# Performance work log

Hardware: AMD Instinct MI355X
Metric: run time of the kernel (lower is better)

## Reference

```python
import jax, jax.numpy as jnp
import numpy as np
from jax import lax

NT, TL = 32, 64           # num_trajs, traj_length
H, W, C = 84, 84, 4       # Atari frame stack
SIZE = 256                # LSTM hidden size
NOUT = 18                 # num_outputs
FEAT = 6 * 6 * 32         # after four stride-2 SAME convs: 84->42->21->11->6
DN = ('NHWC', 'HWIO', 'NHWC')


def setup_inputs() -> dict:
    key = jax.random.key(0)
    ks = jax.random.split(key, 8)
    d = {}
    d['inputs'] = jax.random.normal(ks[0], (NT * TL, H, W, C), jnp.float32)
    cin = C
    for i in range(4):
        d[f'w{i+1}'] = jax.random.normal(ks[1 + i], (3, 3, cin, 32), jnp.float32) * 0.1
        d[f'b{i+1}'] = jnp.zeros((32,), jnp.float32)
        cin = 32
    d['lstm_w'] = jax.random.normal(ks[5], (FEAT + SIZE, 4 * SIZE), jnp.float32) * 0.05
    d['lstm_b'] = jnp.zeros((4 * SIZE,), jnp.float32)
    d['fc_w'] = jax.random.normal(ks[6], (SIZE, NOUT), jnp.float32) * 0.01
    d['fc_b'] = jnp.zeros((NOUT,), jnp.float32)
    d['c0'] = jnp.zeros((NT, SIZE), jnp.float32)
    d['h0'] = jnp.zeros((NT, SIZE), jnp.float32)
    return d


def reference(inputs, w1, b1, w2, b2, w3, b3, w4, b4,
              lstm_w, lstm_b, fc_w, fc_b, c0, h0):
    x = inputs
    for w, b in ((w1, b1), (w2, b2), (w3, b3), (w4, b4)):
        x = jax.nn.elu(lax.conv_general_dilated(
            x, w, window_strides=(2, 2), padding='SAME',
            dimension_numbers=DN) + b)
    # [NT*TL, 6, 6, 32] -> [TL, NT, FEAT] (time-major for scan)
    xs = x.reshape(NT, TL, FEAT).transpose(1, 0, 2)

    def step(carry, xt):
        c, h = carry
        gates = jnp.concatenate([xt, h], axis=-1) @ lstm_w + lstm_b
        i, j, f, o = jnp.split(gates, 4, axis=-1)
        # BasicLSTMCell with forget_bias = 1.0
        new_c = c * jax.nn.sigmoid(f + 1.0) + jax.nn.sigmoid(i) * jnp.tanh(j)
        new_h = jnp.tanh(new_c) * jax.nn.sigmoid(o)
        return (new_c, new_h), new_h

    _, outs = lax.scan(step, (c0, h0), xs)          # outs: [TL, NT, SIZE]
    feats = outs.transpose(1, 0, 2).reshape(-1, SIZE)  # batch-major flatten
    logits = feats @ fc_w + fc_b                    # [NT*TL, NOUT]
    return logits
```

## Files before the change

kernel.cpp:

```cpp
#include <hip/hip_runtime.h>
#include <math.h>

#define NTRAJ 32
#define TLEN  64
#define BATCH (NTRAJ*TLEN)

__device__ __forceinline__ float eluf(float x){ return x > 0.f ? x : expm1f(x); }
__device__ __forceinline__ float sigmf(float x){ return 1.f/(1.f+expf(-x)); }

__global__ __launch_bounds__(256) void conv1_kernel(
    const float* __restrict__ in,
    const float* __restrict__ w,
    const float* __restrict__ b,
    float* __restrict__ out)
{
    int pos = blockIdx.x*256 + threadIdx.x;
    int n   = pos / (42*42);
    int rem = pos % (42*42);
    int oy  = rem / 42, ox = rem % 42;
    float acc[32];
    #pragma unroll
    for(int o=0;o<32;o++) acc[o] = b[o];
    for(int ky=0; ky<3; ky++){
        int iy = 2*oy + ky;
        if(iy >= 84) continue;
        for(int kx=0; kx<3; kx++){
            int ix = 2*ox + kx;
            if(ix >= 84) continue;
            float4 v = *(const float4*)(in + (((n*84 + iy)*84) + ix)*4);
            const float* wq = w + (ky*3 + kx)*128;
            #pragma unroll
            for(int o=0;o<32;o++) acc[o] += v.x*wq[o];
            #pragma unroll
            for(int o=0;o<32;o++) acc[o] += v.y*wq[32+o];
            #pragma unroll
            for(int o=0;o<32;o++) acc[o] += v.z*wq[64+o];
            #pragma unroll
            for(int o=0;o<32;o++) acc[o] += v.w*wq[96+o];
        }
    }
    const int NPOS = BATCH*42*42;
    #pragma unroll
    for(int o=0;o<32;o++) out[o*NPOS + pos] = eluf(acc[o]);
}

template<int IH, int IW, int OH, int OW, int PB>
__global__ __launch_bounds__(256) void convN_kernel(
    const float* __restrict__ in,
    const float* __restrict__ w,
    const float* __restrict__ b,
    float* __restrict__ out)
{
    const int IPLANE = BATCH*IH*IW;
    const int OPLANE = BATCH*OH*OW;
    int pos = blockIdx.x*256 + threadIdx.x;
    if(pos >= OPLANE) return;
    int n   = pos / (OH*OW);
    int rem = pos % (OH*OW);
    int oy  = rem / OW, ox = rem % OW;
    float acc[32];
    #pragma unroll
    for(int o=0;o<32;o++) acc[o] = b[o];
    for(int ky=0; ky<3; ky++){
        int iy = 2*oy + ky - PB;
        if(iy < 0 || iy >= IH) continue;
        for(int kx=0; kx<3; kx++){
            int ix = 2*ox + kx - PB;
            if(ix < 0 || ix >= IW) continue;
            const float* ip = in + (n*IH + iy)*IW + ix;
            const float* wp = w + (ky*3 + kx)*1024;
            for(int ci=0; ci<32; ci+=4){
                float x0 = ip[(ci+0)*IPLANE];
                float x1 = ip[(ci+1)*IPLANE];
                float x2 = ip[(ci+2)*IPLANE];
                float x3 = ip[(ci+3)*IPLANE];
                const float* wq = wp + ci*32;
                #pragma unroll
                for(int o=0;o<32;o++) acc[o] += x0*wq[o];
                #pragma unroll
                for(int o=0;o<32;o++) acc[o] += x1*wq[32+o];
                #pragma unroll
                for(int o=0;o<32;o++) acc[o] += x2*wq[64+o];
                #pragma unroll
                for(int o=0;o<32;o++) acc[o] += x3*wq[96+o];
            }
        }
    }
    #pragma unroll
    for(int o=0;o<32;o++) out[o*OPLANE + pos] = eluf(acc[o]);
}

__global__ __launch_bounds__(256) void relayout_kernel(
    const float* __restrict__ p4,
    float* __restrict__ at)
{
    int i = blockIdx.x*256 + threadIdx.x;
    int f = i >> 11, r = i & 2047;
    int s = f >> 5,  c = f & 31;
    int t = r >> 5,  n = r & 31;
    int nt = n*64 + t;
    at[i] = p4[c*(BATCH*36) + nt*36 + s];
}

__global__ __launch_bounds__(256) void gx_gemm_kernel(
    const float* __restrict__ at,
    const float* __restrict__ lw,
    const float* __restrict__ lb,
    float* __restrict__ gx)
{
    int lane = threadIdx.x & 63;
    int wv   = threadIdx.x >> 6;
    int r0   = blockIdx.x * 16;
    int oc   = blockIdx.y*256 + wv*64 + lane;
    float acc[16];
    float bias = lb[oc];
    #pragma unroll
    for(int i=0;i<16;i++) acc[i] = bias;
    #pragma unroll 4
    for(int k=0;k<1152;k++){
        float wval = lw[k*1024 + oc];
        const float* ap = at + k*2048 + r0;
        #pragma unroll
        for(int i=0;i<16;i++) acc[i] += ap[i] * wval;
    }
    #pragma unroll
    for(int i=0;i<16;i++) gx[(r0+i)*1024 + oc] = acc[i];
}

__global__ __launch_bounds__(256) void lstm_kernel(
    const float* __restrict__ gx,
    const float* __restrict__ lw,
    const float* __restrict__ c0,
    const float* __restrict__ h0,
    float* __restrict__ feats)
{
    __shared__ float hA[256], hB[256], gb[2][1024];
    const float* wh = lw + 1152*1024;
    int t  = threadIdx.x;
    int nA = blockIdx.x*2, nB = nA + 1;
    hA[t] = h0[nA*256 + t];
    hB[t] = h0[nB*256 + t];
    float cA = c0[nA*256 + t];
    float cB = c0[nB*256 + t];
    __syncthreads();
    for(int st=0; st<64; st++){
        float aA0=0.f,aA1=0.f,aA2=0.f,aA3=0.f;
        float aB0=0.f,aB1=0.f,aB2=0.f,aB3=0.f;
        #pragma unroll 4
        for(int k4=0;k4<64;k4++){
            float4 ha = *(const float4*)&hA[k4*4];
            float4 hb = *(const float4*)&hB[k4*4];
            const float* wp = wh + (k4*4)*1024 + 4*t;
            {   float4 w4 = *(const float4*)(wp);
                aA0 += ha.x*w4.x; aA1 += ha.x*w4.y; aA2 += ha.x*w4.z; aA3 += ha.x*w4.w;
                aB0 += hb.x*w4.x; aB1 += hb.x*w4.y; aB2 += hb.x*w4.z; aB3 += hb.x*w4.w; }
            {   float4 w4 = *(const float4*)(wp + 1024);
                aA0 += ha.y*w4.x; aA1 += ha.y*w4.y; aA2 += ha.y*w4.z; aA3 += ha.y*w4.w;
                aB0 += hb.y*w4.x; aB1 += hb.y*w4.y; aB2 += hb.y*w4.z; aB3 += hb.y*w4.w; }
            {   float4 w4 = *(const float4*)(wp + 2048);
                aA0 += ha.z*w4.x; aA1 += ha.z*w4.y; aA2 += ha.z*w4.z; aA3 += ha.z*w4.w;
                aB0 += hb.z*w4.x; aB1 += hb.z*w4.y; aB2 += hb.z*w4.z; aB3 += hb.z*w4.w; }
            {   float4 w4 = *(const float4*)(wp + 3072);
                aA0 += ha.w*w4.x; aA1 += ha.w*w4.y; aA2 += ha.w*w4.z; aA3 += ha.w*w4.w;
                aB0 += hb.w*w4.x; aB1 += hb.w*w4.y; aB2 += hb.w*w4.z; aB3 += hb.w*w4.w; }
        }
        float4 gA = *(const float4*)(gx + (st*32 + nA)*1024 + 4*t);
        float4 gB = *(const float4*)(gx + (st*32 + nB)*1024 + 4*t);
        gb[0][4*t+0] = aA0 + gA.x; gb[0][4*t+1] = aA1 + gA.y;
        gb[0][4*t+2] = aA2 + gA.z; gb[0][4*t+3] = aA3 + gA.w;
        gb[1][4*t+0] = aB0 + gB.x; gb[1][4*t+1] = aB1 + gB.y;
        gb[1][4*t+2] = aB2 + gB.z; gb[1][4*t+3] = aB3 + gB.w;
        __syncthreads();
        {
            float i_ = gb[0][t], j_ = gb[0][t+256], f_ = gb[0][t+512], o_ = gb[0][t+768];
            cA = cA*sigmf(f_+1.f) + sigmf(i_)*tanhf(j_);
            float h = tanhf(cA)*sigmf(o_);
            hA[t] = h;
            feats[(nA*64 + st)*256 + t] = h;
        }
        {
            float i_ = gb[1][t], j_ = gb[1][t+256], f_ = gb[1][t+512], o_ = gb[1][t+768];
            cB = cB*sigmf(f_+1.f) + sigmf(i_)*tanhf(j_);
            float h = tanhf(cB)*sigmf(o_);
            hB[t] = h;
            feats[(nB*64 + st)*256 + t] = h;
        }
        __syncthreads();
    }
}

__global__ __launch_bounds__(64) void fc_kernel(
    const float* __restrict__ feats, const float* __restrict__ fw,
    const float* __restrict__ fb,    float* __restrict__ out)
{
    __shared__ float h[256];
    int p = blockIdx.x, t = threadIdx.x;
    *(float4*)&h[t*4] = *(const float4*)(feats + p*256 + t*4);
    __syncthreads();
    if(t < 18){
        float acc = fb[t];
        for(int k=0;k<256;k++) acc += h[k]*fw[k*18 + t];
        out[p*18 + t] = acc;
    }
}

extern "C" void kernel_launch(void* const* d_in, const int* in_sizes, int n_in,
                              void* d_out, int out_size, void* d_ws, size_t ws_size,
                              hipStream_t stream) {
    const float* inp = (const float*)d_in[0];
    const float* w1  = (const float*)d_in[1];  const float* b1 = (const float*)d_in[2];
    const float* w2  = (const float*)d_in[3];  const float* b2 = (const float*)d_in[4];
    const float* w3  = (const float*)d_in[5];  const float* b3 = (const float*)d_in[6];
    const float* w4  = (const float*)d_in[7];  const float* b4 = (const float*)d_in[8];
    const float* lw  = (const float*)d_in[9];  const float* lb = (const float*)d_in[10];
    const float* fw  = (const float*)d_in[11]; const float* fb = (const float*)d_in[12];
    const float* c0  = (const float*)d_in[13]; const float* h0 = (const float*)d_in[14];
    float* out = (float*)d_out;
    float* ws  = (float*)d_ws;

    const size_t n1 = (size_t)32*3612672;
    const size_t n3 = (size_t)32*247808;
    const size_t n4 = (size_t)32*73728;

    float* p1 = ws;
    float* p2 = p1 + n1;
    float* p3 = ws;
    float* p4 = p3 + n3;
    float* at = p4 + n4;
    float* gxb   = at  + (size_t)1152*2048;
    float* feats = gxb + (size_t)2048*1024;

    conv1_kernel<<<14112,256,0,stream>>>(inp, w1, b1, p1);
    convN_kernel<42,42,21,21,0><<<3528,256,0,stream>>>(p1, w2, b2, p2);
    convN_kernel<21,21,11,11,1><<<968,256,0,stream>>>(p2, w3, b3, p3);
    convN_kernel<11,11, 6, 6,1><<<288,256,0,stream>>>(p3, w4, b4, p4);
    relayout_kernel<<<9216,256,0,stream>>>(p4, at);
    gx_gemm_kernel<<<dim3(128,4),256,0,stream>>>(at, lw, lb, gxb);
    lstm_kernel<<<16,256,0,stream>>>(gxb, lw, c0, h0, feats);
    fc_kernel<<<2048,64,0,stream>>>(feats, fw, fb, out);
}
```

Baseline: 2.067 ms.

## Register-block conv kernels over four positions and keep LSTM weights per-thread

Each conv kernel now stages its weights in shared memory and computes 4 output positions per thread (1 for the last conv). Each weight float4 is reused across those positions, and grid sizes shrink to match. Bounds checks become clamped loads with masked values. The LSTM kernel moves to one trajectory per 1024-thread block, and each thread preloads its 256 recurrent weights into a register array so weights are not re-read from global memory every step. The risks: 256 floats per thread at 1024 threads per block may exceed the register budget and spill to scratch, and only 32 blocks run the LSTM.

```diff
diff --git a/kernel.cpp b/kernel.cpp
--- a/kernel.cpp
+++ b/kernel.cpp
@@ -14,37 +14,60 @@
     const float* __restrict__ b,
     float* __restrict__ out)
 {
-    int pos = blockIdx.x*256 + threadIdx.x;
-    int n   = pos / (42*42);
-    int rem = pos % (42*42);
-    int oy  = rem / 42, ox = rem % 42;
-    float acc[32];
-    #pragma unroll
-    for(int o=0;o<32;o++) acc[o] = b[o];
+    __shared__ float ws[1152];
+    for(int i=threadIdx.x; i<1152; i+=256) ws[i] = w[i];
+    __syncthreads();
+    const int NPOS = BATCH*42*42;
+    int base = blockIdx.x*1024;
+    int n[4], iy0[4], ix0[4];
+    float acc[4][32];
+    #pragma unroll
+    for(int p=0;p<4;p++){
+        int pos = base + p*256 + threadIdx.x;
+        int nn  = pos / (42*42);
+        int rem = pos % (42*42);
+        n[p] = nn; iy0[p] = 2*(rem/42); ix0[p] = 2*(rem%42);
+        #pragma unroll
+        for(int o=0;o<32;o++) acc[p][o] = b[o];
+    }
     for(int ky=0; ky<3; ky++){
-        int iy = 2*oy + ky;
-        if(iy >= 84) continue;
         for(int kx=0; kx<3; kx++){
-            int ix = 2*ox + kx;
-            if(ix >= 84) continue;
-            float4 v = *(const float4*)(in + (((n*84 + iy)*84) + ix)*4);
-            const float* wq = w + (ky*3 + kx)*128;
+            float x[4][4];
             #pragma unroll
-            for(int o=0;o<32;o++) acc[o] += v.x*wq[o];
+            for(int p=0;p<4;p++){
+                int iy = iy0[p]+ky, ix = ix0[p]+kx;
+                bool ok = (iy<84) & (ix<84);
+                int iyc = iy<84?iy:83, ixc = ix<84?ix:83;
+                float4 v = *(const float4*)(in + (((n[p]*84 + iyc)*84) + ixc)*4);
+                x[p][0] = ok ? v.x : 0.f; x[p][1] = ok ? v.y : 0.f;
+                x[p][2] = ok ? v.z : 0.f; x[p][3] = ok ? v.w : 0.f;
+            }
+            const float* wt = ws + (ky*3+kx)*128;
             #pragma unroll
-            for(int o=0;o<32;o++) acc[o] += v.y*wq[32+o];
-            #pragma unroll
-            for(int o=0;o<32;o++) acc[o] += v.z*wq[64+o];
-            #pragma unroll
-            for(int o=0;o<32;o++) acc[o] += v.w*wq[96+o];
-        }
-    }
-    const int NPOS = BATCH*42*42;
-    #pragma unroll
-    for(int o=0;o<32;o++) out[o*NPOS + pos] = eluf(acc[o]);
-}
-
-template<int IH, int IW, int OH, int OW, int PB>
+            for(int q=0;q<4;q++){
+                #pragma unroll
+                for(int o4=0;o4<8;o4++){
+                    float4 w4 = *(const float4*)(wt + q*32 + o4*4);
+                    #pragma unroll
+                    for(int p=0;p<4;p++){
+                        acc[p][o4*4+0] += x[p][q]*w4.x;
+                        acc[p][o4*4+1] += x[p][q]*w4.y;
+                        acc[p][o4*4+2] += x[p][q]*w4.z;
+                        acc[p][o4*4+3] += x[p][q]*w4.w;
+                    }
+                }
+            }
+        }
+    }
+    #pragma unroll
+    for(int p=0;p<4;p++){
+        int pos = base + p*256 + threadIdx.x;
+        #pragma unroll
+        for(int o=0;o<32;o++) out[o*NPOS + pos] = eluf(acc[p][o]);
+    }
+}
+
+template<int IH, int IW, int OH, int OW, int PB, int PX>
 __global__ __launch_bounds__(256) void convN_kernel(
     const float* __restrict__ in,
     const float* __restrict__ w,
@@ -53,41 +76,66 @@
 {
     const int IPLANE = BATCH*IH*IW;
     const int OPLANE = BATCH*OH*OW;
-    int pos = blockIdx.x*256 + threadIdx.x;
-    if(pos >= OPLANE) return;
-    int n   = pos / (OH*OW);
-    int rem = pos % (OH*OW);
-    int oy  = rem / OW, ox = rem % OW;
-    float acc[32];
-    #pragma unroll
-    for(int o=0;o<32;o++) acc[o] = b[o];
+    __shared__ float ws[9216];
+    for(int i=threadIdx.x; i<9216; i+=256) ws[i] = w[i];
+    __syncthreads();
+    int base = blockIdx.x*(256*PX);
+    int n[PX], iy0[PX], ix0[PX];
+    float acc[PX][32];
+    #pragma unroll
+    for(int p=0;p<PX;p++){
+        int pos = base + p*256 + threadIdx.x;
+        int nn  = pos / (OH*OW);
+        int rem = pos % (OH*OW);
+        n[p] = nn; iy0[p] = 2*(rem/OW) - PB; ix0[p] = 2*(rem%OW) - PB;
+        #pragma unroll
+        for(int o=0;o<32;o++) acc[p][o] = b[o];
+    }
     for(int ky=0; ky<3; ky++){
-        int iy = 2*oy + ky - PB;
-        if(iy < 0 || iy >= IH) continue;
         for(int kx=0; kx<3; kx++){
-            int ix = 2*ox + kx - PB;
-            if(ix < 0 || ix >= IW) continue;
-            const float* ip = in + (n*IH + iy)*IW + ix;
-            const float* wp = w + (ky*3 + kx)*1024;
+            const float* wt = ws + (ky*3+kx)*1024;
+            const float* ipb[PX]; bool okm[PX];
+            #pragma unroll
+            for(int p=0;p<PX;p++){
+                int iy = iy0[p]+ky, ix = ix0[p]+kx;
+                okm[p] = (iy>=0) & (iy<IH) & (ix>=0) & (ix<IW);
+                int iyc = iy<0?0:(iy>=IH?IH-1:iy);
+                int ixc = ix<0?0:(ix>=IW?IW-1:ix);
+                ipb[p] = in + (n[p]*IH + iyc)*IW + ixc;
+            }
             for(int ci=0; ci<32; ci+=4){
-                float x0 = ip[(ci+0)*IPLANE];
-                float x1 = ip[(ci+1)*IPLANE];
-                float x2 = ip[(ci+2)*IPLANE];
-                float x3 = ip[(ci+3)*IPLANE];
-                const float* wq = wp + ci*32;
+                float x[PX][4];
                 #pragma unroll
-                for(int o=0;o<32;o++) acc[o] += x0*wq[o];
+                for(int p=0;p<PX;p++){
+                    #pragma unroll
+                    for(int q=0;q<4;q++){
+                        float v = ipb[p][(ci+q)*IPLANE];
+                        x[p][q] = okm[p] ? v : 0.f;
+                    }
+                }
                 #pragma unroll
-                for(int o=0;o<32;o++) acc[o] += x1*wq[32+o];
-                #pragma unroll
-                for(int o=0;o<32;o++) acc[o] += x2*wq[64+o];
-                #pragma unroll
-                for(int o=0;o<32;o++) acc[o] += x3*wq[96+o];
-            }
-        }
-    }
-    #pragma unroll
-    for(int o=0;o<32;o++) out[o*OPLANE + pos] = eluf(acc[o]);
+                for(int q=0;q<4;q++){
+                    #pragma unroll
+                    for(int o4=0;o4<8;o4++){
+                        float4 w4 = *(const float4*)(wt + (ci+q)*32 + o4*4);
+                        #pragma unroll
+                        for(int p=0;p<PX;p++){
+                            acc[p][o4*4+0] += x[p][q]*w4.x;
+                            acc[p][o4*4+1] += x[p][q]*w4.y;
+                            acc[p][o4*4+2] += x[p][q]*w4.z;
+                            acc[p][o4*4+3] += x[p][q]*w4.w;
+                        }
+                    }
+                }
+            }
+        }
+    }
+    #pragma unroll
+    for(int p=0;p<PX;p++){
+        int pos = base + p*256 + threadIdx.x;
+        #pragma unroll
+        for(int o=0;o<32;o++) out[o*OPLANE + pos] = eluf(acc[p][o]);
+    }
 }
 
 __global__ __launch_bounds__(256) void relayout_kernel(
@@ -127,63 +175,43 @@
     for(int i=0;i<16;i++) gx[(r0+i)*1024 + oc] = acc[i];
 }
 
-__global__ __launch_bounds__(256) void lstm_kernel(
+__global__ __launch_bounds__(1024) void lstm_kernel(
     const float* __restrict__ gx,
     const float* __restrict__ lw,
     const float* __restrict__ c0,
     const float* __restrict__ h0,
     float* __restrict__ feats)
 {
-    __shared__ float hA[256], hB[256], gb[2][1024];
+    __shared__ float hs[256];
+    __shared__ float gb[1024];
+    const int t = threadIdx.x;
+    const int n = blockIdx.x;
     const float* wh = lw + 1152*1024;
-    int t  = threadIdx.x;
-    int nA = blockIdx.x*2, nB = nA + 1;
-    hA[t] = h0[nA*256 + t];
-    hB[t] = h0[nB*256 + t];
-    float cA = c0[nA*256 + t];
-    float cB = c0[nB*256 + t];
+    float w[256];
+    #pragma unroll
+    for(int k=0;k<256;k++) w[k] = wh[k*1024 + t];
+    if(t < 256) hs[t] = h0[n*256 + t];
+    float c = (t < 256) ? c0[n*256 + t] : 0.f;
     __syncthreads();
     for(int st=0; st<64; st++){
-        float aA0=0.f,aA1=0.f,aA2=0.f,aA3=0.f;
-        float aB0=0.f,aB1=0.f,aB2=0.f,aB3=0.f;
-        #pragma unroll 4
+        float g = gx[(st*32 + n)*1024 + t];
+        float a0=0.f, a1=0.f, a2=0.f, a3=0.f;
+        #pragma unroll
         for(int k4=0;k4<64;k4++){
-            float4 ha = *(const float4*)&hA[k4*4];
-            float4 hb = *(const float4*)&hB[k4*4];
-            const float* wp = wh + (k4*4)*1024 + 4*t;
-            {   float4 w4 = *(const float4*)(wp);
-                aA0 += ha.x*w4.x; aA1 += ha.x*w4.y; aA2 += ha.x*w4.z; aA3 += ha.x*w4.w;
-                aB0 += hb.x*w4.x; aB1 += hb.x*w4.y; aB2 += hb.x*w4.z; aB3 += hb.x*w4.w; }
-            {   float4 w4 = *(const float4*)(wp + 1024);
-                aA0 += ha.y*w4.x; aA1 += ha.y*w4.y; aA2 += ha.y*w4.z; aA3 += ha.y*w4.w;
-                aB0 += hb.y*w4.x; aB1 += hb.y*w4.y; aB2 += hb.y*w4.z; aB3 += hb.y*w4.w; }
-            {   float4 w4 = *(const float4*)(wp + 2048);
-                aA0 += ha.z*w4.x; aA1 += ha.z*w4.y; aA2 += ha.z*w4.z; aA3 += ha.z*w4.w;
-                aB0 += hb.z*w4.x; aB1 += hb.z*w4.y; aB2 += hb.z*w4.z; aB3 += hb.z*w4.w; }
-            {   float4 w4 = *(const float4*)(wp + 3072);
-                aA0 += ha.w*w4.x; aA1 += ha.w*w4.y; aA2 += ha.w*w4.z; aA3 += ha.w*w4.w;
-                aB0 += hb.w*w4.x; aB1 += hb.w*w4.y; aB2 += hb.w*w4.z; aB3 += hb.w*w4.w; }
-        }
-        float4 gA = *(const float4*)(gx + (st*32 + nA)*1024 + 4*t);
-        float4 gB = *(const float4*)(gx + (st*32 + nB)*1024 + 4*t);
-        gb[0][4*t+0] = aA0 + gA.x; gb[0][4*t+1] = aA1 + gA.y;
-        gb[0][4*t+2] = aA2 + gA.z; gb[0][4*t+3] = aA3 + gA.w;
-        gb[1][4*t+0] = aB0 + gB.x; gb[1][4*t+1] = aB1 + gB.y;
-        gb[1][4*t+2] = aB2 + gB.z; gb[1][4*t+3] = aB3 + gB.w;
+            float4 h4 = *(const float4*)&hs[k4*4];
+            a0 += h4.x*w[4*k4+0];
+            a1 += h4.y*w[4*k4+1];
+            a2 += h4.z*w[4*k4+2];
+            a3 += h4.w*w[4*k4+3];
+        }
+        gb[t] = (a0+a1)+(a2+a3) + g;
         __syncthreads();
-        {
-            float i_ = gb[0][t], j_ = gb[0][t+256], f_ = gb[0][t+512], o_ = gb[0][t+768];
-            cA = cA*sigmf(f_+1.f) + sigmf(i_)*tanhf(j_);
-            float h = tanhf(cA)*sigmf(o_);
-            hA[t] = h;
-            feats[(nA*64 + st)*256 + t] = h;
-        }
-        {
-            float i_ = gb[1][t], j_ = gb[1][t+256], f_ = gb[1][t+512], o_ = gb[1][t+768];
-            cB = cB*sigmf(f_+1.f) + sigmf(i_)*tanhf(j_);
-            float h = tanhf(cB)*sigmf(o_);
-            hB[t] = h;
-            feats[(nB*64 + st)*256 + t] = h;
+        if(t < 256){
+            float i_ = gb[t], j_ = gb[t+256], f_ = gb[t+512], o_ = gb[t+768];
+            c = c*sigmf(f_+1.f) + sigmf(i_)*tanhf(j_);
+            float h = tanhf(c)*sigmf(o_);
+            hs[t] = h;
+            feats[(n*64 + st)*256 + t] = h;
         }
         __syncthreads();
     }
@@ -230,12 +258,12 @@
     float* gxb   = at  + (size_t)1152*2048;
     float* feats = gxb + (size_t)2048*1024;
 
-    conv1_kernel<<<14112,256,0,stream>>>(inp, w1, b1, p1);
-    convN_kernel<42,42,21,21,0><<<3528,256,0,stream>>>(p1, w2, b2, p2);
-    convN_kernel<21,21,11,11,1><<<968,256,0,stream>>>(p2, w3, b3, p3);
-    convN_kernel<11,11, 6, 6,1><<<288,256,0,stream>>>(p3, w4, b4, p4);
+    conv1_kernel<<<3528,256,0,stream>>>(inp, w1, b1, p1);
+    convN_kernel<42,42,21,21,0,4><<<882,256,0,stream>>>(p1, w2, b2, p2);
+    convN_kernel<21,21,11,11,1,4><<<242,256,0,stream>>>(p2, w3, b3, p3);
+    convN_kernel<11,11, 6, 6,1,1><<<288,256,0,stream>>>(p3, w4, b4, p4);
     relayout_kernel<<<9216,256,0,stream>>>(p4, at);
     gx_gemm_kernel<<<dim3(128,4),256,0,stream>>>(at, lw, lb, gxb);
-    lstm_kernel<<<16,256,0,stream>>>(gxb, lw, c0, h0, feats);
+    lstm_kernel<<<32,1024,0,stream>>>(gxb, lw, c0, h0, feats);
     fc_kernel<<<2048,64,0,stream>>>(feats, fw, fb, out);
 }
```

Result: slower. 3.156 ms (+52.7%).

## Split LSTM recurrence across 32 cooperative blocks with register-resident weights and grid sync

Applied to the files above, without the earlier changes.

The recurrent LSTM kernel used to run as 16 blocks, each handling two trajectories and streaming the full 256x1024 recurrent weight matrix from global memory at every step. Now 32 cooperative blocks each own 8 hidden units (32 gate columns) for all trajectories. Each block keeps its weight slice in registers, reads the whole hidden state from a double-buffered global buffer, reduces partial sums through shuffles and shared memory, and synchronizes the grid once per step. This removes the repeated weight traffic but adds a grid-wide barrier and a global hidden-state exchange on each of the 64 steps.

```diff
diff --git a/kernel.cpp b/kernel.cpp
--- a/kernel.cpp
+++ b/kernel.cpp
@@ -1,5 +1,8 @@
 #include <hip/hip_runtime.h>
+#include <hip/hip_cooperative_groups.h>
 #include <math.h>
+
+namespace cg = cooperative_groups;
 
 #define NTRAJ 32
 #define TLEN  64
@@ -132,60 +135,85 @@
     const float* __restrict__ lw,
     const float* __restrict__ c0,
     const float* __restrict__ h0,
-    float* __restrict__ feats)
-{
-    __shared__ float hA[256], hB[256], gb[2][1024];
+    float* __restrict__ feats,
+    float* __restrict__ hbuf)
+{
+    cg::grid_group grid = cg::this_grid();
+    __shared__ float h_s[8192];
+    __shared__ float part[4][32][33];
+    __shared__ float gatef[32][32];
+    const int t    = threadIdx.x;
+    const int wg   = blockIdx.x;
+    const int col16= t & 15;
+    const int kseg = t >> 4;
+    const int lane = t & 63;
+    const int wv   = t >> 6;
     const float* wh = lw + 1152*1024;
-    int t  = threadIdx.x;
-    int nA = blockIdx.x*2, nB = nA + 1;
-    hA[t] = h0[nA*256 + t];
-    hB[t] = h0[nB*256 + t];
-    float cA = c0[nA*256 + t];
-    float cB = c0[nB*256 + t];
-    __syncthreads();
+
+    const int gAc = ((col16>>3)<<8)      + wg*8 + (col16&7);
+    const int gBc = (((col16+16)>>3)<<8) + wg*8 + ((col16+16)&7);
+
+    float wAr[16], wBr[16];
+    #pragma unroll
+    for(int j=0;j<16;j++){
+        wAr[j] = wh[(kseg*16+j)*1024 + gAc];
+        wBr[j] = wh[(kseg*16+j)*1024 + gBc];
+    }
+    const int cn = t & 31, cu = t >> 5;
+    const int uglob = wg*8 + cu;
+    float c = c0[cn*256 + uglob];
+    hbuf[wg*256 + t] = h0[wg*256 + t];
+    __threadfence();
+    grid.sync();
+
     for(int st=0; st<64; st++){
-        float aA0=0.f,aA1=0.f,aA2=0.f,aA3=0.f;
-        float aB0=0.f,aB1=0.f,aB2=0.f,aB3=0.f;
+        const float* hsrc = hbuf + (st&1)*8192;
+        #pragma unroll
+        for(int r=0;r<8;r++){
+            int off = r*1024 + t*4;
+            *(float4*)&h_s[off] = *(const float4*)&hsrc[off];
+        }
+        __syncthreads();
         #pragma unroll 4
-        for(int k4=0;k4<64;k4++){
-            float4 ha = *(const float4*)&hA[k4*4];
-            float4 hb = *(const float4*)&hB[k4*4];
-            const float* wp = wh + (k4*4)*1024 + 4*t;
-            {   float4 w4 = *(const float4*)(wp);
-                aA0 += ha.x*w4.x; aA1 += ha.x*w4.y; aA2 += ha.x*w4.z; aA3 += ha.x*w4.w;
-                aB0 += hb.x*w4.x; aB1 += hb.x*w4.y; aB2 += hb.x*w4.z; aB3 += hb.x*w4.w; }
-            {   float4 w4 = *(const float4*)(wp + 1024);
-                aA0 += ha.y*w4.x; aA1 += ha.y*w4.y; aA2 += ha.y*w4.z; aA3 += ha.y*w4.w;
-                aB0 += hb.y*w4.x; aB1 += hb.y*w4.y; aB2 += hb.y*w4.z; aB3 += hb.y*w4.w; }
-            {   float4 w4 = *(const float4*)(wp + 2048);
-                aA0 += ha.z*w4.x; aA1 += ha.z*w4.y; aA2 += ha.z*w4.z; aA3 += ha.z*w4.w;
-                aB0 += hb.z*w4.x; aB1 += hb.z*w4.y; aB2 += hb.z*w4.z; aB3 += hb.z*w4.w; }
-            {   float4 w4 = *(const float4*)(wp + 3072);
-                aA0 += ha.w*w4.x; aA1 += ha.w*w4.y; aA2 += ha.w*w4.z; aA3 += ha.w*w4.w;
-                aB0 += hb.w*w4.x; aB1 += hb.w*w4.y; aB2 += hb.w*w4.z; aB3 += hb.w*w4.w; }
-        }
-        float4 gA = *(const float4*)(gx + (st*32 + nA)*1024 + 4*t);
-        float4 gB = *(const float4*)(gx + (st*32 + nB)*1024 + 4*t);
-        gb[0][4*t+0] = aA0 + gA.x; gb[0][4*t+1] = aA1 + gA.y;
-        gb[0][4*t+2] = aA2 + gA.z; gb[0][4*t+3] = aA3 + gA.w;
-        gb[1][4*t+0] = aB0 + gB.x; gb[1][4*t+1] = aB1 + gB.y;
-        gb[1][4*t+2] = aB2 + gB.z; gb[1][4*t+3] = aB3 + gB.w;
+        for(int n=0;n<32;n++){
+            const float4* hp = (const float4*)&h_s[n*256 + kseg*16];
+            float4 ha = hp[0], hb = hp[1], hc = hp[2], hd = hp[3];
+            float pA = ha.x*wAr[0]  + ha.y*wAr[1]  + ha.z*wAr[2]  + ha.w*wAr[3]
+                     + hb.x*wAr[4]  + hb.y*wAr[5]  + hb.z*wAr[6]  + hb.w*wAr[7]
+                     + hc.x*wAr[8]  + hc.y*wAr[9]  + hc.z*wAr[10] + hc.w*wAr[11]
+                     + hd.x*wAr[12] + hd.y*wAr[13] + hd.z*wAr[14] + hd.w*wAr[15];
+            float pB = ha.x*wBr[0]  + ha.y*wBr[1]  + ha.z*wBr[2]  + ha.w*wBr[3]
+                     + hb.x*wBr[4]  + hb.y*wBr[5]  + hb.z*wBr[6]  + hb.w*wBr[7]
+                     + hc.x*wBr[8]  + hc.y*wBr[9]  + hc.z*wBr[10] + hc.w*wBr[11]
+                     + hd.x*wBr[12] + hd.y*wBr[13] + hd.z*wBr[14] + hd.w*wBr[15];
+            pA += __shfl_xor(pA, 16, 64);
+            pA += __shfl_xor(pA, 32, 64);
+            pB += __shfl_xor(pB, 16, 64);
+            pB += __shfl_xor(pB, 32, 64);
+            if(lane < 16){
+                part[wv][n][lane]    = pA;
+                part[wv][n][lane+16] = pB;
+            }
+        }
         __syncthreads();
-        {
-            float i_ = gb[0][t], j_ = gb[0][t+256], f_ = gb[0][t+512], o_ = gb[0][t+768];
-            cA = cA*sigmf(f_+1.f) + sigmf(i_)*tanhf(j_);
-            float h = tanhf(cA)*sigmf(o_);
-            hA[t] = h;
-            feats[(nA*64 + st)*256 + t] = h;
-        }
-        {
-            float i_ = gb[1][t], j_ = gb[1][t+256], f_ = gb[1][t+512], o_ = gb[1][t+768];
-            cB = cB*sigmf(f_+1.f) + sigmf(i_)*tanhf(j_);
-            float h = tanhf(cB)*sigmf(o_);
-            hB[t] = h;
-            feats[(nB*64 + st)*256 + t] = h;
+        #pragma unroll
+        for(int e=0;e<4;e++){
+            int idx  = t + e*256;
+            int n    = idx & 31, colX = idx >> 5;
+            int cg_  = ((colX>>3)<<8) + wg*8 + (colX&7);
+            float s  = part[0][n][colX] + part[1][n][colX]
+                     + part[2][n][colX] + part[3][n][colX];
+            gatef[colX][n] = s + gx[(st*32 + n)*1024 + cg_];
         }
         __syncthreads();
+        float i_ = gatef[cu][cn],    j_ = gatef[8+cu][cn],
+              f_ = gatef[16+cu][cn], o_ = gatef[24+cu][cn];
+        c = c*sigmf(f_+1.f) + sigmf(i_)*tanhf(j_);
+        float h = tanhf(c)*sigmf(o_);
+        hbuf[((st+1)&1)*8192 + cn*256 + uglob] = h;
+        feats[(cn*64 + st)*256 + uglob] = h;
+        __threadfence();
+        grid.sync();
     }
 }
 
@@ -229,6 +257,7 @@
     float* at = p4 + n4;
     float* gxb   = at  + (size_t)1152*2048;
     float* feats = gxb + (size_t)2048*1024;
+    float* hbuf  = feats + (size_t)2048*256;
 
     conv1_kernel<<<14112,256,0,stream>>>(inp, w1, b1, p1);
     convN_kernel<42,42,21,21,0><<<3528,256,0,stream>>>(p1, w2, b2, p2);
@@ -236,6 +265,11 @@
     convN_kernel<11,11, 6, 6,1><<<288,256,0,stream>>>(p3, w4, b4, p4);
     relayout_kernel<<<9216,256,0,stream>>>(p4, at);
     gx_gemm_kernel<<<dim3(128,4),256,0,stream>>>(at, lw, lb, gxb);
-    lstm_kernel<<<16,256,0,stream>>>(gxb, lw, c0, h0, feats);
+    {
+        void* args[] = { (void*)&gxb, (void*)&lw, (void*)&c0, (void*)&h0,
+                         (void*)&feats, (void*)&hbuf };
+        hipLaunchCooperativeKernel((void*)lstm_kernel, dim3(32), dim3(256),
+                                   args, 0, stream);
+    }
     fc_kernel<<<2048,64,0,stream>>>(feats, fw, fb, out);
 }
```

New measurement: 2.523 ms. 1.22x slower.
